# Optimization experiments

Hardware: AMD Instinct MI355X
Metric: run time of the kernel (lower is better)

## Reference

```python
import jax, jax.numpy as jnp
import numpy as np

N = 100_000      # nodes
E = 1_600_000    # edges (avg degree 16)
IN, HID, OUT = 256, 256, 128  # in_dim, 2*out_dim, out_dim
BN_EPS = 1e-5


def setup_inputs() -> dict:
    key = jax.random.key(0)
    ks = jax.random.split(key, 8)
    x = jax.random.normal(ks[0], (N, IN), jnp.float32)
    edge_index = jax.random.randint(ks[1], (2, E), 0, N, dtype=jnp.int64)
    # GCNConv weights (glorot-ish scaling) + biases
    W1 = jax.random.normal(ks[2], (IN, HID), jnp.float32) * (1.0 / np.sqrt(IN))
    b1 = jnp.zeros((HID,), jnp.float32)
    W2 = jax.random.normal(ks[3], (HID, OUT), jnp.float32) * (1.0 / np.sqrt(HID))
    b2 = jnp.zeros((OUT,), jnp.float32)
    # BatchNorm1d affine params
    gamma = jnp.ones((HID,), jnp.float32)
    beta = jnp.zeros((HID,), jnp.float32)
    # PReLU single learnable slope (torch default 0.25)
    a = jnp.full((1,), 0.25, jnp.float32)
    return {"x": x, "edge_index": edge_index, "W1": W1, "b1": b1,
            "W2": W2, "b2": b2, "gamma": gamma, "beta": beta, "a": a}


def gcn_layer(x, W, b, src, dst):
    """GCNConv: h = D^-1/2 (A + I) D^-1/2 (x @ W) + b, self-loop weight 1."""
    h = x @ W                                           # [N, F]
    deg = jnp.zeros((N,), h.dtype).at[dst].add(1.0) + 1.0  # +1 self-loop
    dinv = jax.lax.rsqrt(deg)                           # [N]
    norm = dinv[src] * dinv[dst]                        # [E]
    agg = jnp.zeros_like(h).at[dst].add(h[src] * norm[:, None])
    agg = agg + h * (dinv * dinv)[:, None]              # self-loop term
    return agg + b


def reference(x, edge_index, W1, b1, W2, b2, gamma, beta, a):
    src, dst = edge_index[0], edge_index[1]
    h = gcn_layer(x, W1, b1, src, dst)                  # [N, HID]
    # BatchNorm1d (training mode: batch statistics, biased var)
    mean = jnp.mean(h, axis=0)
    var = jnp.var(h, axis=0)
    h = (h - mean) * jax.lax.rsqrt(var + BN_EPS) * gamma + beta
    # PReLU with single shared slope
    h = jnp.where(h > 0, h, a * h)
    return gcn_layer(h, W2, b2, src, dst)               # [N, OUT]
```

## Files before the change

### kernel.cpp

```cpp
#include <hip/hip_runtime.h>
#include <hip/hip_bf16.h>
#include <stdint.h>

#define IN_DIM 256

typedef __attribute__((ext_vector_type(8))) short short8;
typedef __attribute__((ext_vector_type(4))) float f32x4;

__device__ __forceinline__ float bf2f(unsigned short u){
  return __uint_as_float(((unsigned int)u) << 16);
}
__device__ __forceinline__ unsigned short f2bf(float f){
  unsigned int u = __float_as_uint(f);
  u = u + 0x7FFFu + ((u >> 16) & 1u);
  return (unsigned short)(u >> 16);
}

#if __has_builtin(__builtin_amdgcn_cvt_f32_ubyte0)
__device__ __forceinline__ float ub0(uint v){ return __builtin_amdgcn_cvt_f32_ubyte0(v); }
__device__ __forceinline__ float ub1(uint v){ return __builtin_amdgcn_cvt_f32_ubyte1(v); }
__device__ __forceinline__ float ub2(uint v){ return __builtin_amdgcn_cvt_f32_ubyte2(v); }
__device__ __forceinline__ float ub3(uint v){ return __builtin_amdgcn_cvt_f32_ubyte3(v); }
#else
__device__ __forceinline__ float ub0(uint v){ return (float)(v & 0xFF); }
__device__ __forceinline__ float ub1(uint v){ return (float)((v >> 8) & 0xFF); }
__device__ __forceinline__ float ub2(uint v){ return (float)((v >> 16) & 0xFF); }
__device__ __forceinline__ float ub3(uint v){ return (float)(v >> 24); }
#endif

__global__ void k_detect(const void* ei, long long E, int N, int* flag){
  __shared__ int bad;
  if (threadIdx.x == 0) bad = 0;
  __syncthreads();
  const long long* p = (const long long*)ei;
  long long stride = E / 1024; if (stride < 1) stride = 1;
  for (int i = threadIdx.x; i < 1024; i += blockDim.x){
    long long idx = (long long)i * stride;
    if (idx >= E) break;
    long long v = p[idx];
    if (v < 0 || v >= (long long)N) atomicOr(&bad, 1);
  }
  __syncthreads();
  if (threadIdx.x == 0) flag[0] = bad ? 0 : 1;
}

__device__ __forceinline__ int edge_at(const void* ei, long long i, int f64){
  if (f64) return (int)((const long long*)ei)[i];
  return ((const int*)ei)[i];
}

__global__ void k_hist(const void* ei, long long E, const int* flag, int* cnt){
  long long e = (long long)blockIdx.x * blockDim.x + threadIdx.x;
  if (e < E){
    int f = flag[0];
    int d = edge_at(ei, E + e, f);
    atomicAdd(&cnt[d], 1);
  }
}

__global__ void k_scan1(const int* cnt, int* rs, int* bsum, float* dinv, int* fill, int N){
  __shared__ int sh[1024];
  int i = blockIdx.x * 1024 + threadIdx.x;
  int v = (i < N) ? cnt[i] : 0;
  sh[threadIdx.x] = v;
  __syncthreads();
  for (int o = 1; o < 1024; o <<= 1){
    int x = (threadIdx.x >= o) ? sh[threadIdx.x - o] : 0;
    __syncthreads();
    sh[threadIdx.x] += x;
    __syncthreads();
  }
  if (i < N){
    rs[i] = sh[threadIdx.x] - v;
    dinv[i] = rsqrtf((float)v + 1.0f);
    fill[i] = 0;
  }
  if (threadIdx.x == 1023) bsum[blockIdx.x] = sh[1023];
}

__global__ void k_scan2(const int* bsum, int* boff, int nb, int* rs, int N,
                        float* sums, float* sqs){
  __shared__ int sh[128];
  int t = threadIdx.x;
  int v = (t < nb) ? bsum[t] : 0;
  sh[t] = v;
  __syncthreads();
  for (int o = 1; o < 128; o <<= 1){
    int x = (t >= o) ? sh[t - o] : 0;
    __syncthreads();
    sh[t] += x;
    __syncthreads();
  }
  boff[t] = sh[t] - v;
  if (t == 127) rs[N] = sh[127];
  sums[t] = 0.f; sums[t + 128] = 0.f;
  sqs[t]  = 0.f; sqs[t + 128]  = 0.f;
}

__global__ void k_scan3(int* rs, const int* boff, int N){
  int i = blockIdx.x * 1024 + threadIdx.x;
  if (i < N) rs[i] += boff[blockIdx.x];
}

__global__ void k_scatter(const void* ei, long long E, const int* flag, const int* rs,
                          int* fill, int* csrc){
  long long e = (long long)blockIdx.x * blockDim.x + threadIdx.x;
  if (e < E){
    int f = flag[0];
    int s = edge_at(ei, e, f);
    int d = edge_at(ei, E + e, f);
    int pos = atomicAdd(&fill[d], 1);
    csrc[rs[d] + pos] = s;
  }
}

__global__ void k_prep(const float* __restrict__ x, ushort* __restrict__ xb,
                       const float* __restrict__ W1, ushort* __restrict__ W1t,
                       const float* __restrict__ W2, ushort* __restrict__ W2t,
                       int N, int NP){
  int idx = blockIdx.x * 256 + threadIdx.x;
  int nxq = NP * 64;
  if (idx < nxq){
    int row = idx >> 6, q = idx & 63;
    ushort4 o = {0, 0, 0, 0};
    if (row < N){
      float4 v = ((const float4*)x)[(size_t)row * 64 + q];
      o.x = f2bf(v.x); o.y = f2bf(v.y); o.z = f2bf(v.z); o.w = f2bf(v.w);
    }
    ((ushort4*)xb)[idx] = o;
  } else {
    int j = idx - nxq;
    if (j < 256 * 256){
      int n = j >> 8, k = j & 255;
      W1t[j] = f2bf(W1[(size_t)k * 256 + n]);
    } else {
      j -= 65536;
      if (j < 128 * 256){
        int n = j >> 8, k = j & 255;
        W2t[j] = f2bf(W2[(size_t)k * 128 + n]);
      }
    }
  }
}

__global__ __launch_bounds__(256) void k_gemm(const ushort* __restrict__ A,
                                              const ushort* __restrict__ Bt,
                                              ushort* __restrict__ C,
                                              const float* __restrict__ dinv,
                                              int N, int Nc){
  __shared__ ushort As[128 * 64];
  __shared__ ushort Bs[128 * 64];
  const int tid = threadIdx.x;
  const int wave = tid >> 6, lane = tid & 63;
  const long long row0 = (long long)blockIdx.x * 128;
  const int col0 = blockIdx.y * 128;
  const int lr = lane >> 3, lc = lane & 7;
  const int mrow = ((wave & 1) << 6) + (lane & 15);
  const int ncol = ((wave >> 1) << 6) + (lane & 15);

  f32x4 acc[4][4];
  #pragma unroll
  for (int i = 0; i < 4; ++i)
    #pragma unroll
    for (int j = 0; j < 4; ++j)
      acc[i][j] = (f32x4){0.f, 0.f, 0.f, 0.f};

  const ushort* gA = A + (row0 + wave * 32 + lr) * 256 + lc * 8;
  const ushort* gB = Bt + ((long long)(col0 + wave * 32 + lr)) * 256 + lc * 8;
  ushort* lA = As + wave * 2048;
  ushort* lB = Bs + wave * 2048;

  #pragma unroll
  for (int kt = 0; kt < 4; ++kt){
    #pragma unroll
    for (int i = 0; i < 4; ++i){
      __builtin_amdgcn_global_load_lds(
          (const __attribute__((address_space(1))) void*)(gA + kt * 64 + i * 8 * 256),
          (__attribute__((address_space(3))) void*)(lA + i * 512), 16, 0, 0);
      __builtin_amdgcn_global_load_lds(
          (const __attribute__((address_space(1))) void*)(gB + kt * 64 + i * 8 * 256),
          (__attribute__((address_space(3))) void*)(lB + i * 512), 16, 0, 0);
    }
    __syncthreads();
    #pragma unroll
    for (int ks = 0; ks < 2; ++ks){
      const int kb = ks * 32 + ((lane >> 4) << 3);
      short8 af[4], bfv[4];
      #pragma unroll
      for (int i = 0; i < 4; ++i) af[i] = *(const short8*)(As + (mrow + i * 16) * 64 + kb);
      #pragma unroll
      for (int j = 0; j < 4; ++j) bfv[j] = *(const short8*)(Bs + (ncol + j * 16) * 64 + kb);
      #pragma unroll
      for (int i = 0; i < 4; ++i)
        #pragma unroll
        for (int j = 0; j < 4; ++j)
          acc[i][j] = __builtin_amdgcn_mfma_f32_16x16x32_bf16(af[i], bfv[j], acc[i][j], 0, 0, 0);
    }
    __syncthreads();
  }

  const int rbase = ((wave & 1) << 6) + ((lane >> 4) << 2);
  const int cb = col0 + ((wave >> 1) << 6) + (lane & 15);
  #pragma unroll
  for (int i = 0; i < 4; ++i)
    #pragma unroll
    for (int r = 0; r < 4; ++r){
      long long row = row0 + rbase + i * 16 + r;
      float sc = (row < N) ? dinv[row] : 0.f;
      #pragma unroll
      for (int j = 0; j < 4; ++j)
        C[row * Nc + cb + j * 16] = f2bf(sc * acc[i][j][r]);
    }
}

__global__ __launch_bounds__(256) void k_quant1(const ushort* __restrict__ hb,
    uint* __restrict__ q, float* __restrict__ sc, int N){
  int lane = threadIdx.x & 63;
  int r = blockIdx.x * 4 + (threadIdx.x >> 6);
  if (r >= N) return;
  ushort4 v = ((const ushort4*)hb)[(size_t)r * 64 + lane];
  float f0 = bf2f(v.x), f1 = bf2f(v.y), f2 = bf2f(v.z), f3 = bf2f(v.w);
  float m = fmaxf(fmaxf(fabsf(f0), fabsf(f1)), fmaxf(fabsf(f2), fabsf(f3)));
  #pragma unroll
  for (int o = 32; o >= 1; o >>= 1) m = fmaxf(m, __shfl_xor(m, o, 64));
  float scale = m * (1.0f / 127.0f);
  float inv = (m > 0.f) ? 127.0f / m : 0.f;
  uint b0 = (uint)(int)(rintf(f0 * inv) + 128.0f);
  uint b1 = (uint)(int)(rintf(f1 * inv) + 128.0f);
  uint b2 = (uint)(int)(rintf(f2 * inv) + 128.0f);
  uint b3 = (uint)(int)(rintf(f3 * inv) + 128.0f);
  q[(size_t)r * 64 + lane] = b0 | (b1 << 8) | (b2 << 16) | (b3 << 24);
  if (lane == 0) sc[r] = scale;
}

__global__ __launch_bounds__(256) void k_quant2(const ushort* __restrict__ hb,
    ushort* __restrict__ q, float* __restrict__ sc, int N){
  int lane = threadIdx.x & 63;
  int r = blockIdx.x * 4 + (threadIdx.x >> 6);
  if (r >= N) return;
  uint v = ((const uint*)hb)[(size_t)r * 64 + lane];
  float f0 = bf2f((unsigned short)(v & 0xFFFF));
  float f1 = bf2f((unsigned short)(v >> 16));
  float m = fmaxf(fabsf(f0), fabsf(f1));
  #pragma unroll
  for (int o = 32; o >= 1; o >>= 1) m = fmaxf(m, __shfl_xor(m, o, 64));
  float scale = m * (1.0f / 127.0f);
  float inv = (m > 0.f) ? 127.0f / m : 0.f;
  uint b0 = (uint)(int)(rintf(f0 * inv) + 128.0f);
  uint b1 = (uint)(int)(rintf(f1 * inv) + 128.0f);
  q[(size_t)r * 64 + lane] = (ushort)(b0 | (b1 << 8));
  if (lane == 0) sc[r] = scale;
}

__global__ __launch_bounds__(256) void k_agg1(const uint* __restrict__ q, const float* __restrict__ sc,
    const int* __restrict__ rs, const int* __restrict__ csrc, const float* __restrict__ b1,
    ushort* __restrict__ h1, float* __restrict__ sums, float* __restrict__ sqs,
    int N, int nblocks){
  __shared__ float red[4 * 512];
  const int lane = threadIdx.x & 63;
  const int wid = (blockIdx.x * 256 + threadIdx.x) >> 6;
  const int nw = (nblocks * 256) >> 6;
  const float4 bb = ((const float4*)b1)[lane];
  float st0 = 0.f, st1 = 0.f, st2 = 0.f, st3 = 0.f;
  float sq0 = 0.f, sq1 = 0.f, sq2 = 0.f, sq3 = 0.f;

  for (int n = wid; n < N; n += nw){
    int e = rs[n], end = rs[n + 1];
    float dn = rsqrtf((float)(end - e) + 1.0f);
    float scn = sc[n];
    uint v = q[(size_t)n * 64 + lane];
    float ssum = scn;
    float a0 = scn * ub0(v), a1 = scn * ub1(v), a2 = scn * ub2(v), a3 = scn * ub3(v);
    for (; e + 4 <= end; e += 4){
      int s0 = csrc[e], s1 = csrc[e + 1], s2 = csrc[e + 2], s3 = csrc[e + 3];
      float c0 = sc[s0], c1 = sc[s1], c2 = sc[s2], c3 = sc[s3];
      uint v0 = q[(size_t)s0 * 64 + lane];
      uint v1 = q[(size_t)s1 * 64 + lane];
      uint v2 = q[(size_t)s2 * 64 + lane];
      uint v3 = q[(size_t)s3 * 64 + lane];
      ssum += (c0 + c1) + (c2 + c3);
      a0 += (c0 * ub0(v0) + c1 * ub0(v1)) + (c2 * ub0(v2) + c3 * ub0(v3));
      a1 += (c0 * ub1(v0) + c1 * ub1(v1)) + (c2 * ub1(v2) + c3 * ub1(v3));
      a2 += (c0 * ub2(v0) + c1 * ub2(v1)) + (c2 * ub2(v2) + c3 * ub2(v3));
      a3 += (c0 * ub3(v0) + c1 * ub3(v1)) + (c2 * ub3(v2) + c3 * ub3(v3));
    }
    for (; e < end; ++e){
      int s = csrc[e];
      float c = sc[s];
      uint vv = q[(size_t)s * 64 + lane];
      ssum += c;
      a0 += c * ub0(vv); a1 += c * ub1(vv); a2 += c * ub2(vv); a3 += c * ub3(vv);
    }
    float corr = -128.0f * ssum;
    float h0 = dn * (a0 + corr) + bb.x;
    float h1v = dn * (a1 + corr) + bb.y;
    float h2 = dn * (a2 + corr) + bb.z;
    float h3 = dn * (a3 + corr) + bb.w;
    st0 += h0; st1 += h1v; st2 += h2; st3 += h3;
    sq0 += h0 * h0; sq1 += h1v * h1v; sq2 += h2 * h2; sq3 += h3 * h3;
    ushort4 o;
    o.x = f2bf(h0); o.y = f2bf(h1v); o.z = f2bf(h2); o.w = f2bf(h3);
    ((ushort4*)h1)[(size_t)n * 64 + lane] = o;
  }

  int wv = threadIdx.x >> 6;
  int f = lane * 4;
  red[wv * 512 + f]     = st0; red[wv * 512 + f + 1] = st1;
  red[wv * 512 + f + 2] = st2; red[wv * 512 + f + 3] = st3;
  __syncthreads();
  float v0s = red[threadIdx.x] + red[512 + threadIdx.x] + red[1024 + threadIdx.x] + red[1536 + threadIdx.x];
  float v1s = (threadIdx.x < 256) ? 0.f : 0.f;
  __syncthreads();
  red[wv * 512 + f]     = sq0; red[wv * 512 + f + 1] = sq1;
  red[wv * 512 + f + 2] = sq2; red[wv * 512 + f + 3] = sq3;
  __syncthreads();
  float v0q = red[threadIdx.x] + red[512 + threadIdx.x] + red[1024 + threadIdx.x] + red[1536 + threadIdx.x];
  (void)v1s;
  if (threadIdx.x < 256){
    atomicAdd(&sums[threadIdx.x], v0s);
    atomicAdd(&sqs[threadIdx.x], v0q);
  }
}

__global__ __launch_bounds__(256) void k_agg2(const ushort* __restrict__ q, const float* __restrict__ sc,
    const int* __restrict__ rs, const int* __restrict__ csrc, const float* __restrict__ b2,
    float* __restrict__ out, int N, int nblocks){
  const int lane = threadIdx.x & 63;
  const int wid = (blockIdx.x * 256 + threadIdx.x) >> 6;
  const int nw = (nblocks * 256) >> 6;
  const float2 bb = ((const float2*)b2)[lane];

  for (int n = wid; n < N; n += nw){
    int e = rs[n], end = rs[n + 1];
    float dn = rsqrtf((float)(end - e) + 1.0f);
    float scn = sc[n];
    uint v = (uint)q[(size_t)n * 64 + lane];
    float ssum = scn;
    float a0 = scn * ub0(v), a1 = scn * ub1(v);
    for (; e + 4 <= end; e += 4){
      int s0 = csrc[e], s1 = csrc[e + 1], s2 = csrc[e + 2], s3 = csrc[e + 3];
      float c0 = sc[s0], c1 = sc[s1], c2 = sc[s2], c3 = sc[s3];
      uint v0 = (uint)q[(size_t)s0 * 64 + lane];
      uint v1 = (uint)q[(size_t)s1 * 64 + lane];
      uint v2 = (uint)q[(size_t)s2 * 64 + lane];
      uint v3 = (uint)q[(size_t)s3 * 64 + lane];
      ssum += (c0 + c1) + (c2 + c3);
      a0 += (c0 * ub0(v0) + c1 * ub0(v1)) + (c2 * ub0(v2) + c3 * ub0(v3));
      a1 += (c0 * ub1(v0) + c1 * ub1(v1)) + (c2 * ub1(v2) + c3 * ub1(v3));
    }
    for (; e < end; ++e){
      int s = csrc[e];
      float c = sc[s];
      uint vv = (uint)q[(size_t)s * 64 + lane];
      ssum += c;
      a0 += c * ub0(vv); a1 += c * ub1(vv);
    }
    float corr = -128.0f * ssum;
    float2 r;
    r.x = dn * (a0 + corr) + bb.x;
    r.y = dn * (a1 + corr) + bb.y;
    ((float2*)out)[(size_t)n * 64 + lane] = r;
  }
}

__global__ void k_prelu(const ushort* __restrict__ h1, const float* __restrict__ sums,
                        const float* __restrict__ sqs, const float* __restrict__ gamma,
                        const float* __restrict__ beta, const float* __restrict__ aP,
                        ushort* __restrict__ P, int N, int NP){
  int idx = blockIdx.x * 256 + threadIdx.x;
  int row = idx >> 7, cp = idx & 127;
  if (row >= NP) return;
  uint o = 0;
  if (row < N){
    int c0 = 2 * cp;
    float inv = 1.0f / (float)N;
    float m0 = sums[c0] * inv,     m1 = sums[c0 + 1] * inv;
    float v0 = sqs[c0] * inv - m0 * m0, v1 = sqs[c0 + 1] * inv - m1 * m1;
    float sc0 = gamma[c0] * rsqrtf(v0 + 1e-5f);
    float sc1 = gamma[c0 + 1] * rsqrtf(v1 + 1e-5f);
    float sh0 = beta[c0] - m0 * sc0;
    float sh1 = beta[c0 + 1] - m1 * sc1;
    uint v = ((const uint*)h1)[(size_t)row * 128 + cp];
    float aa = aP[0];
    float x0 = bf2f((unsigned short)(v & 0xFFFF)) * sc0 + sh0;
    float x1 = bf2f((unsigned short)(v >> 16)) * sc1 + sh1;
    x0 = x0 > 0.f ? x0 : aa * x0;
    x1 = x1 > 0.f ? x1 : aa * x1;
    o = (uint)f2bf(x0) | ((uint)f2bf(x1) << 16);
  }
  ((uint*)P)[idx] = o;
}

extern "C" void kernel_launch(void* const* d_in, const int* in_sizes, int n_in,
                              void* d_out, int out_size, void* d_ws, size_t ws_size,
                              hipStream_t stream){
  const float* x  = (const float*)d_in[0];
  const void*  ei = d_in[1];
  const float* W1 = (const float*)d_in[2];
  const float* b1 = (const float*)d_in[3];
  const float* W2 = (const float*)d_in[4];
  const float* b2 = (const float*)d_in[5];
  const float* gm = (const float*)d_in[6];
  const float* bt = (const float*)d_in[7];
  const float* aP = (const float*)d_in[8];
  float* out = (float*)d_out;

  const int N = in_sizes[0] / IN_DIM;
  const long long E = in_sizes[1] / 2;
  const int NP = ((N + 127) / 128) * 128;

  char* w = (char*)d_ws;
  size_t off = 0;
  auto carve = [&](size_t bytes) -> char* {
    char* p = w + off;
    off += (bytes + 255) & ~(size_t)255;
    return p;
  };
  ushort* xb  = (ushort*)carve((size_t)NP * 256 * 2);
  ushort* hb  = (ushort*)carve((size_t)NP * 256 * 2);
  ushort* h1b = (ushort*)carve((size_t)NP * 256 * 2);
  ushort* W1t = (ushort*)carve(256 * 256 * 2);
  ushort* W2t = (ushort*)carve(128 * 256 * 2);
  int*   cnt  = (int*)  carve((size_t)N * 4);
  int*   rs   = (int*)  carve((size_t)(N + 1) * 4);
  int*   fill = (int*)  carve((size_t)N * 4);
  int*   csrc = (int*)  carve((size_t)E * 4);
  float* dinv = (float*)carve((size_t)N * 4);
  float* sc1  = (float*)carve((size_t)N * 4);
  float* sc2  = (float*)carve((size_t)N * 4);
  int*   bsum = (int*)  carve(512);
  int*   boff = (int*)  carve(512);
  float* sums = (float*)carve(1024);
  float* sqs  = (float*)carve(1024);
  int*   flag = (int*)  carve(256);
  uint*   q8a = (uint*)xb;
  ushort* q8b = (ushort*)h1b;

  const int NB1 = (N + 1023) / 1024;
  const int egrid = (int)((E + 255) / 256);
  const int prep_grid = (NP * 64 + 256 * 256 + 128 * 256 + 255) / 256;
  const int AGG1_BLOCKS = 1024, AGG2_BLOCKS = 2048;

  k_detect<<<1, 256, 0, stream>>>(ei, E, N, flag);
  hipMemsetAsync(cnt, 0, (size_t)N * 4, stream);
  k_prep<<<prep_grid, 256, 0, stream>>>(x, xb, W1, W1t, W2, W2t, N, NP);
  k_hist<<<egrid, 256, 0, stream>>>(ei, E, flag, cnt);
  k_scan1<<<NB1, 1024, 0, stream>>>(cnt, rs, bsum, dinv, fill, N);
  k_scan2<<<1, 128, 0, stream>>>(bsum, boff, NB1, rs, N, sums, sqs);
  k_scan3<<<NB1, 1024, 0, stream>>>(rs, boff, N);
  k_scatter<<<egrid, 256, 0, stream>>>(ei, E, flag, rs, fill, csrc);

  k_gemm<<<dim3(NP / 128, 2), 256, 0, stream>>>(xb, W1t, hb, dinv, N, 256);
  k_quant1<<<(N + 3) / 4, 256, 0, stream>>>(hb, q8a, sc1, N);
  k_agg1<<<AGG1_BLOCKS, 256, 0, stream>>>(q8a, sc1, rs, csrc, b1, h1b, sums, sqs, N, AGG1_BLOCKS);
  k_prelu<<<(NP * 128 + 255) / 256, 256, 0, stream>>>(h1b, sums, sqs, gm, bt, aP, xb, N, NP);
  k_gemm<<<dim3(NP / 128, 1), 256, 0, stream>>>(xb, W2t, hb, dinv, N, 128);
  k_quant2<<<(N + 3) / 4, 256, 0, stream>>>(hb, q8b, sc2, N);
  k_agg2<<<AGG2_BLOCKS, 256, 0, stream>>>(q8b, sc2, rs, csrc, b2, out, N, AGG2_BLOCKS);
}
```

Measured before the change: 638.5 us.

## Split quantized feature rows into column planes and vectorize edge index loads

The int8 quantized feature tables are stored as four (layer 1) or two (layer 2) column planes instead of row-major, so each 64-byte gathered segment comes from its own smaller plane, which may improve cache locality for random neighbor gathers. The aggregation loops peel edges until the index is 4-aligned and then load four source indices with one int4 load. The agg1 grid is doubled. The gather count is unchanged, so any benefit depends on cache behaviour of the planar layout.

```diff
diff --git a/kernel.cpp b/kernel.cpp
--- a/kernel.cpp
+++ b/kernel.cpp
@@ -214,7 +214,7 @@
 }
 
 __global__ __launch_bounds__(256) void k_quant1(const ushort* __restrict__ hb,
-    uint* __restrict__ q, float* __restrict__ sc, int N){
+    uint* __restrict__ q, float* __restrict__ sc, int N, int PL){
   int lane = threadIdx.x & 63;
   int r = blockIdx.x * 4 + (threadIdx.x >> 6);
   if (r >= N) return;
@@ -229,12 +229,13 @@
   uint b1 = (uint)(int)(rintf(f1 * inv) + 128.0f);
   uint b2 = (uint)(int)(rintf(f2 * inv) + 128.0f);
   uint b3 = (uint)(int)(rintf(f3 * inv) + 128.0f);
-  q[(size_t)r * 64 + lane] = b0 | (b1 << 8) | (b2 << 16) | (b3 << 24);
+  q[(size_t)(lane >> 4) * PL + (size_t)r * 16 + (lane & 15)] =
+      b0 | (b1 << 8) | (b2 << 16) | (b3 << 24);
   if (lane == 0) sc[r] = scale;
 }
 
 __global__ __launch_bounds__(256) void k_quant2(const ushort* __restrict__ hb,
-    ushort* __restrict__ q, float* __restrict__ sc, int N){
+    ushort* __restrict__ q, float* __restrict__ sc, int N, int PL2){
   int lane = threadIdx.x & 63;
   int r = blockIdx.x * 4 + (threadIdx.x >> 6);
   if (r >= N) return;
@@ -248,19 +249,20 @@
   float inv = (m > 0.f) ? 127.0f / m : 0.f;
   uint b0 = (uint)(int)(rintf(f0 * inv) + 128.0f);
   uint b1 = (uint)(int)(rintf(f1 * inv) + 128.0f);
-  q[(size_t)r * 64 + lane] = (ushort)(b0 | (b1 << 8));
+  q[(size_t)(lane >> 5) * PL2 + (size_t)r * 32 + (lane & 31)] = (ushort)(b0 | (b1 << 8));
   if (lane == 0) sc[r] = scale;
 }
 
 __global__ __launch_bounds__(256) void k_agg1(const uint* __restrict__ q, const float* __restrict__ sc,
     const int* __restrict__ rs, const int* __restrict__ csrc, const float* __restrict__ b1,
     ushort* __restrict__ h1, float* __restrict__ sums, float* __restrict__ sqs,
-    int N, int nblocks){
+    int N, int nblocks, int PL){
   __shared__ float red[4 * 512];
   const int lane = threadIdx.x & 63;
   const int wid = (blockIdx.x * 256 + threadIdx.x) >> 6;
   const int nw = (nblocks * 256) >> 6;
   const float4 bb = ((const float4*)b1)[lane];
+  const uint* qb = q + (size_t)(lane >> 4) * PL + (lane & 15);
   float st0 = 0.f, st1 = 0.f, st2 = 0.f, st3 = 0.f;
   float sq0 = 0.f, sq1 = 0.f, sq2 = 0.f, sq3 = 0.f;
 
@@ -268,16 +270,23 @@
     int e = rs[n], end = rs[n + 1];
     float dn = rsqrtf((float)(end - e) + 1.0f);
     float scn = sc[n];
-    uint v = q[(size_t)n * 64 + lane];
+    uint v = qb[(size_t)n * 16];
     float ssum = scn;
     float a0 = scn * ub0(v), a1 = scn * ub1(v), a2 = scn * ub2(v), a3 = scn * ub3(v);
+    for (; e < end && (e & 3); ++e){
+      int s = csrc[e];
+      float c = sc[s];
+      uint vv = qb[(size_t)s * 16];
+      ssum += c;
+      a0 += c * ub0(vv); a1 += c * ub1(vv); a2 += c * ub2(vv); a3 += c * ub3(vv);
+    }
     for (; e + 4 <= end; e += 4){
-      int s0 = csrc[e], s1 = csrc[e + 1], s2 = csrc[e + 2], s3 = csrc[e + 3];
-      float c0 = sc[s0], c1 = sc[s1], c2 = sc[s2], c3 = sc[s3];
-      uint v0 = q[(size_t)s0 * 64 + lane];
-      uint v1 = q[(size_t)s1 * 64 + lane];
-      uint v2 = q[(size_t)s2 * 64 + lane];
-      uint v3 = q[(size_t)s3 * 64 + lane];
+      int4 s4 = *(const int4*)(csrc + e);
+      float c0 = sc[s4.x], c1 = sc[s4.y], c2 = sc[s4.z], c3 = sc[s4.w];
+      uint v0 = qb[(size_t)s4.x * 16];
+      uint v1 = qb[(size_t)s4.y * 16];
+      uint v2 = qb[(size_t)s4.z * 16];
+      uint v3 = qb[(size_t)s4.w * 16];
       ssum += (c0 + c1) + (c2 + c3);
       a0 += (c0 * ub0(v0) + c1 * ub0(v1)) + (c2 * ub0(v2) + c3 * ub0(v3));
       a1 += (c0 * ub1(v0) + c1 * ub1(v1)) + (c2 * ub1(v2) + c3 * ub1(v3));
@@ -287,7 +296,7 @@
     for (; e < end; ++e){
       int s = csrc[e];
       float c = sc[s];
-      uint vv = q[(size_t)s * 64 + lane];
+      uint vv = qb[(size_t)s * 16];
       ssum += c;
       a0 += c * ub0(vv); a1 += c * ub1(vv); a2 += c * ub2(vv); a3 += c * ub3(vv);
     }
@@ -309,13 +318,11 @@
   red[wv * 512 + f + 2] = st2; red[wv * 512 + f + 3] = st3;
   __syncthreads();
   float v0s = red[threadIdx.x] + red[512 + threadIdx.x] + red[1024 + threadIdx.x] + red[1536 + threadIdx.x];
-  float v1s = (threadIdx.x < 256) ? 0.f : 0.f;
   __syncthreads();
   red[wv * 512 + f]     = sq0; red[wv * 512 + f + 1] = sq1;
   red[wv * 512 + f + 2] = sq2; red[wv * 512 + f + 3] = sq3;
   __syncthreads();
   float v0q = red[threadIdx.x] + red[512 + threadIdx.x] + red[1024 + threadIdx.x] + red[1536 + threadIdx.x];
-  (void)v1s;
   if (threadIdx.x < 256){
     atomicAdd(&sums[threadIdx.x], v0s);
     atomicAdd(&sqs[threadIdx.x], v0q);
@@ -324,26 +331,34 @@
 
 __global__ __launch_bounds__(256) void k_agg2(const ushort* __restrict__ q, const float* __restrict__ sc,
     const int* __restrict__ rs, const int* __restrict__ csrc, const float* __restrict__ b2,
-    float* __restrict__ out, int N, int nblocks){
+    float* __restrict__ out, int N, int nblocks, int PL2){
   const int lane = threadIdx.x & 63;
   const int wid = (blockIdx.x * 256 + threadIdx.x) >> 6;
   const int nw = (nblocks * 256) >> 6;
   const float2 bb = ((const float2*)b2)[lane];
+  const ushort* qb = q + (size_t)(lane >> 5) * PL2 + (lane & 31);
 
   for (int n = wid; n < N; n += nw){
     int e = rs[n], end = rs[n + 1];
     float dn = rsqrtf((float)(end - e) + 1.0f);
     float scn = sc[n];
-    uint v = (uint)q[(size_t)n * 64 + lane];
+    uint v = (uint)qb[(size_t)n * 32];
     float ssum = scn;
     float a0 = scn * ub0(v), a1 = scn * ub1(v);
+    for (; e < end && (e & 3); ++e){
+      int s = csrc[e];
+      float c = sc[s];
+      uint vv = (uint)qb[(size_t)s * 32];
+      ssum += c;
+      a0 += c * ub0(vv); a1 += c * ub1(vv);
+    }
     for (; e + 4 <= end; e += 4){
-      int s0 = csrc[e], s1 = csrc[e + 1], s2 = csrc[e + 2], s3 = csrc[e + 3];
-      float c0 = sc[s0], c1 = sc[s1], c2 = sc[s2], c3 = sc[s3];
-      uint v0 = (uint)q[(size_t)s0 * 64 + lane];
-      uint v1 = (uint)q[(size_t)s1 * 64 + lane];
-      uint v2 = (uint)q[(size_t)s2 * 64 + lane];
-      uint v3 = (uint)q[(size_t)s3 * 64 + lane];
+      int4 s4 = *(const int4*)(csrc + e);
+      float c0 = sc[s4.x], c1 = sc[s4.y], c2 = sc[s4.z], c3 = sc[s4.w];
+      uint v0 = (uint)qb[(size_t)s4.x * 32];
+      uint v1 = (uint)qb[(size_t)s4.y * 32];
+      uint v2 = (uint)qb[(size_t)s4.z * 32];
+      uint v3 = (uint)qb[(size_t)s4.w * 32];
       ssum += (c0 + c1) + (c2 + c3);
       a0 += (c0 * ub0(v0) + c1 * ub0(v1)) + (c2 * ub0(v2) + c3 * ub0(v3));
       a1 += (c0 * ub1(v0) + c1 * ub1(v1)) + (c2 * ub1(v2) + c3 * ub1(v3));
@@ -351,7 +366,7 @@
     for (; e < end; ++e){
       int s = csrc[e];
       float c = sc[s];
-      uint vv = (uint)q[(size_t)s * 64 + lane];
+      uint vv = (uint)qb[(size_t)s * 32];
       ssum += c;
       a0 += c * ub0(vv); a1 += c * ub1(vv);
     }
@@ -408,6 +423,8 @@
   const int N = in_sizes[0] / IN_DIM;
   const long long E = in_sizes[1] / 2;
   const int NP = ((N + 127) / 128) * 128;
+  const int PL  = NP * 16;
+  const int PL2 = NP * 32;
 
   char* w = (char*)d_ws;
   size_t off = 0;
@@ -439,7 +456,7 @@
   const int NB1 = (N + 1023) / 1024;
   const int egrid = (int)((E + 255) / 256);
   const int prep_grid = (NP * 64 + 256 * 256 + 128 * 256 + 255) / 256;
-  const int AGG1_BLOCKS = 1024, AGG2_BLOCKS = 2048;
+  const int AGG1_BLOCKS = 2048, AGG2_BLOCKS = 2048;
 
   k_detect<<<1, 256, 0, stream>>>(ei, E, N, flag);
   hipMemsetAsync(cnt, 0, (size_t)N * 4, stream);
@@ -451,10 +468,10 @@
   k_scatter<<<egrid, 256, 0, stream>>>(ei, E, flag, rs, fill, csrc);
 
   k_gemm<<<dim3(NP / 128, 2), 256, 0, stream>>>(xb, W1t, hb, dinv, N, 256);
-  k_quant1<<<(N + 3) / 4, 256, 0, stream>>>(hb, q8a, sc1, N);
-  k_agg1<<<AGG1_BLOCKS, 256, 0, stream>>>(q8a, sc1, rs, csrc, b1, h1b, sums, sqs, N, AGG1_BLOCKS);
+  k_quant1<<<(N + 3) / 4, 256, 0, stream>>>(hb, q8a, sc1, N, PL);
+  k_agg1<<<AGG1_BLOCKS, 256, 0, stream>>>(q8a, sc1, rs, csrc, b1, h1b, sums, sqs, N, AGG1_BLOCKS, PL);
   k_prelu<<<(NP * 128 + 255) / 256, 256, 0, stream>>>(h1b, sums, sqs, gm, bt, aP, xb, N, NP);
   k_gemm<<<dim3(NP / 128, 1), 256, 0, stream>>>(xb, W2t, hb, dinv, N, 128);
-  k_quant2<<<(N + 3) / 4, 256, 0, stream>>>(hb, q8b, sc2, N);
-  k_agg2<<<AGG2_BLOCKS, 256, 0, stream>>>(q8b, sc2, rs, csrc, b2, out, N, AGG2_BLOCKS);
-}
+  k_quant2<<<(N + 3) / 4, 256, 0, stream>>>(hb, q8b, sc2, N, PL2);
+  k_agg2<<<AGG2_BLOCKS, 256, 0, stream>>>(q8b, sc2, rs, csrc, b2, out, N, AGG2_BLOCKS, PL2);
+}
```

New measurement: 682.5 us. +6.9%, slower.
